# Kernel tuning notes

Hardware: AMD Instinct MI355X
Metric: run time of the kernel (lower is better)

The kernel has to match this reference:

```python
import jax, jax.numpy as jnp
import numpy as np

NHEAD = 8
TOPKS = [16, 8]  # coarse -> fine (indexed by loop i over reversed pyramids)


def _gather_kv(t, idx):
    # t: [b, M, nh, d], idx: [b, N, K, nh] -> gathered [b, N, K, nh, d]
    b, M, nh, d = t.shape
    bi = jnp.arange(b)[:, None, None, None]
    hi = jnp.arange(nh)[None, None, None, :]
    return t[bi, idx, hi]


def _process_level(query, key, value, topk_pos, topk_prev, topk):
    # query: [b, c, h0, w0]; key/value: [b, c, h1, w1] with h1=h0, w1=w0
    bs, c, h0, w0 = query.shape
    _, _, h1, w1 = key.shape
    nh = NHEAD
    d = c // nh
    N = (h0 // 2) * (w0 // 2)
    # b c h w -> b (h w) nh d
    k = key.reshape(bs, c, h1 * w1).transpose(0, 2, 1).reshape(bs, h1 * w1, nh, d)
    v = value.reshape(bs, c, h1 * w1).transpose(0, 2, 1).reshape(bs, h1 * w1, nh, d)
    # b c (h 2) (w 2) -> b (h w) 4 nh d  (2x2 query groups)
    q = query.reshape(bs, c, h0 // 2, 2, w0 // 2, 2)
    q = q.transpose(0, 2, 4, 3, 5, 1).reshape(bs, N, 4, nh, d)
    # expand each coarse candidate position into its 2x2 children in the key grid
    tp = topk_pos * 2  # [2, b, N, Kp, nh]
    idx = jnp.stack([(tp[0] + x) * w1 + (tp[1] + y)
                     for x in (0, 1) for y in (0, 1)], axis=3)  # [b,N,Kp,4,nh]
    K = topk_prev * 4
    idx = idx.reshape(bs, N, K, nh)
    # sparse scores: QK[b,n,t,k,h] = <q[b,n,t,h,:], key[b, idx[b,n,k,h], h, :]>
    kg = _gather_kv(k, idx)  # [b,N,K,nh,d]
    QK = jnp.einsum('bnthd,bnkhd->bntkh', q, kg) * (d ** -0.5)
    A = jax.nn.softmax(QK, axis=-2)  # softmax over the K candidates
    # top-k over candidates (dim=-2 of A); lax.top_k works on last axis
    A_t = jnp.swapaxes(A, -1, -2)  # [b,N,4,nh,K]
    ts_t, li = jax.lax.top_k(A_t, topk)
    idx_bc = jnp.broadcast_to(jnp.swapaxes(idx, -1, -2)[:, :, None], A_t.shape)
    ti_t = jnp.take_along_axis(idx_bc, li, axis=-1)
    topk_score = jnp.swapaxes(ts_t, -1, -2)  # [b,N,4,topk,nh]
    topk_idx = jnp.swapaxes(ti_t, -1, -2)
    # value aggregation (idx is repeated over the 4 group slots in the original,
    # so a single gather is the same math): message[b,n,t,h,d]=sum_k A*v[idx]
    vg = _gather_kv(v, idx)  # [b,N,K,nh,d]
    message = jnp.einsum('bntkh,bnkhd->bnthd', A, vg)  # [b,N,4,nh,d]

    def regroup(x):  # b (h w) (t1 t2) k nh -> b (h t1 w t2) k nh
        x = x.reshape(bs, h0 // 2, w0 // 2, 2, 2, topk, nh)
        return x.transpose(0, 1, 3, 2, 4, 5, 6).reshape(bs, h0 * w0, topk, nh)

    return message, regroup(topk_score), regroup(topk_idx)


def _forward(q_fine, q_coarse, k_fine, k_coarse, v_fine, v_coarse, weight, topk_pos):
    queries = [q_fine, q_coarse]  # original list order: fine -> coarse
    keys = [k_fine, k_coarse]
    values = [v_fine, v_coarse]
    messages = []
    topk = TOPKS[0]
    tp = topk_pos
    for i, (q, k, v) in enumerate(zip(queries[::-1], keys[::-1], values[::-1])):
        w1 = k.shape[3]
        topk_prev, topk = topk, TOPKS[i]
        msg, ts, ti = _process_level(q, k, v, tp, topk_prev, topk)
        messages.append(msg)
        tp = jnp.stack([ti // w1, ti % w1])  # (row, col) in current key grid
    wsm = jax.nn.softmax(weight)

    def comb(x, H):  # b (H W) (t1 t2) h d -> b (H t1 W t2) h d, t1=t2=2
        bs, N, _, nh, d = x.shape
        W = N // H
        x = x.reshape(bs, H, W, 2, 2, nh, d).transpose(0, 1, 3, 2, 4, 5, 6)
        return x.reshape(bs, H * 2 * W * 2, nh, d)

    fm = None
    for i, m in enumerate(messages):
        if i == 0:
            fm = m * wsm[i]
        else:
            fm = fm[:, :, None] + m * wsm[i]
        # faithful to original: queries[-i] (note queries[-0] == queries[0])
        H = queries[-i].shape[2]
        fm = comb(fm, H)
    return fm  # [b, Hf*Wf, nh, d]


def setup_inputs() -> dict:
    key = jax.random.key(0)
    ks = jax.random.split(key, 8)
    f = jnp.float32
    return {
        'q_fine': jax.random.normal(ks[0], (2, 128, 128, 128), f),
        'q_coarse': jax.random.normal(ks[1], (2, 128, 64, 64), f),
        'k_fine': jax.random.normal(ks[2], (2, 128, 128, 128), f),
        'k_coarse': jax.random.normal(ks[3], (2, 128, 64, 64), f),
        'v_fine': jax.random.normal(ks[4], (2, 128, 128, 128), f),
        'v_coarse': jax.random.normal(ks[5], (2, 128, 64, 64), f),
        'weight': jax.random.normal(ks[6], (2,), f),
        'topk_pos': jax.random.randint(ks[7], (2, 2, 1024, 16, 8), 0, 32, dtype=jnp.int32),
    }


def reference(q_fine, q_coarse, k_fine, k_coarse, v_fine, v_coarse, weight, topk_pos):
    return _forward(q_fine, q_coarse, k_fine, k_coarse, v_fine, v_coarse, weight, topk_pos)
```

## Files before the change

kernel.cpp:

```cpp
#include <hip/hip_runtime.h>

#define C 128

__device__ __forceinline__ void wave_sync() {
  __builtin_amdgcn_wave_barrier();
  asm volatile("s_waitcnt lgkmcnt(0)" ::: "memory");
  __builtin_amdgcn_wave_barrier();
}

__device__ __forceinline__ void transpose_tile(const float* __restrict__ in,
                                               float* __restrict__ out, int P,
                                               int tx, int chHalf, int b,
                                               float (*tile)[65]) {
  int posBase = tx * 64;
  int chBase  = chHalf * 64;
  int tid = threadIdx.x;
  int lp = tid & 63;
  int lr = tid >> 6;
  const float* ip = in + (size_t)b * C * P;
  float* op = out + (size_t)b * C * P;
#pragma unroll
  for (int it = 0; it < 16; ++it) {
    int ch = lr + it * 4;
    tile[ch][lp] = ip[(size_t)(chBase + ch) * P + posBase + lp];
  }
  __syncthreads();
  int ch2 = chBase + lp;
  int hh = ch2 >> 4, dd = ch2 & 15;
#pragma unroll
  for (int it = 0; it < 16; ++it) {
    int pl = lr + it * 4;
    op[((size_t)hh * P + posBase + pl) * 16 + dd] = tile[lp][pl];
  }
}

__global__ __launch_bounds__(256) void transpose_coarse(
    const float* __restrict__ q, const float* __restrict__ k,
    const float* __restrict__ v, float* __restrict__ qo,
    float* __restrict__ ko, float* __restrict__ vo) {
  __shared__ alignas(16) float tile[64][65];
  int idx = blockIdx.x;
  int tx = idx & 63;
  int ty = (idx >> 6) % 6;
  int tz = idx / 384;
  int sel = ty >> 1;
  const float* in = sel == 0 ? q : sel == 1 ? k : v;
  float* out      = sel == 0 ? qo : sel == 1 ? ko : vo;
  transpose_tile(in, out, 4096, tx, ty & 1, tz, tile);
}

__global__ __launch_bounds__(256) void fused_mid(
    const float* __restrict__ qf, const float* __restrict__ kf,
    const float* __restrict__ vf, float* __restrict__ qtf,
    float* __restrict__ ktf, float* __restrict__ vtf,
    const float* __restrict__ qt, const float* __restrict__ kt,
    const float* __restrict__ vt, const int* __restrict__ parents,
    float* __restrict__ mc, int* __restrict__ ti_out)
{
  __shared__ alignas(16) float lds[64 * 65];

  if (blockIdx.x < 3072) {
    int idx = blockIdx.x;
    int tx = idx & 255;
    int ty = (idx >> 8) % 6;
    int tz = idx / 1536;
    int sel = ty >> 1;
    const float* in = sel == 0 ? qf : sel == 1 ? kf : vf;
    float* out      = sel == 0 ? qtf : sel == 1 ? ktf : vtf;
    transpose_tile(in, out, 16384, tx, ty & 1, tz, (float (*)[65])lds);
    return;
  }

  float (*als_t)[4][64]    = (float (*)[4][64])   lds;
  float (*als_k)[4][17][4] = (float (*)[4][17][4])(lds + 1024);
  float (*qls)[4][16]      = (float (*)[4][16])  (lds + 2112);
  int   (*cofs)[64]        = (int (*)[64])       (lds + 2368);

  const int abid = blockIdx.x - 3072;
  const int lane = threadIdx.x & 63;
  const int wid  = threadIdx.x >> 6;
  const int wg = (abid & 7) * 512 + (abid >> 3);
  const int u  = wg * 4 + wid;
  const int h  = u & 7;
  const int bn = u >> 3;
  const int n  = bn & 1023;
  const int b  = bn >> 10;
  const int hb = n >> 5;
  const int wb = n & 31;
  const int hD = h * 16;
  const int bh = b * 8 + h;

  { int t = lane >> 4, dd = lane & 15;
    int pix = (hb * 2 + (t >> 1)) * 64 + (wb * 2 + (t & 1));
    qls[wid][t][dd] = qt[((size_t)bh * 4096 + pix) * 16 + dd]; }
  int cand, off0;
  { int kp = lane >> 2, c = lane & 3;
    int r  = parents[(size_t)b * 131072          + n * 128 + kp * 8 + h];
    int cc = parents[(size_t)b * 131072 + 262144 + n * 128 + kp * 8 + h];
    cand = (2 * r + (c >> 1)) * 64 + 2 * cc + (c & 1);
    off0 = (bh * 4096 + cand) * 16;
    cofs[wid][lane] = off0; }
  wave_sync();

  const float4* kv4 = (const float4*)(kt + off0);
  float4 k0 = kv4[0], k1 = kv4[1], k2 = kv4[2], k3 = kv4[3];
  float sc[4];
#pragma unroll
  for (int t = 0; t < 4; ++t) {
    const float4* qv = (const float4*)qls[wid][t];
    float4 q0 = qv[0], q1 = qv[1], q2 = qv[2], q3 = qv[3];
    float acc = k0.x*q0.x + k0.y*q0.y + k0.z*q0.z + k0.w*q0.w
              + k1.x*q1.x + k1.y*q1.y + k1.z*q1.z + k1.w*q1.w
              + k2.x*q2.x + k2.y*q2.y + k2.z*q2.z + k2.w*q2.w
              + k3.x*q3.x + k3.y*q3.y + k3.z*q3.z + k3.w*q3.w;
    sc[t] = acc * 0.25f;
  }

  float mx[4], ex[4], sm[4], a[4];
#pragma unroll
  for (int t = 0; t < 4; ++t) mx[t] = sc[t];
#pragma unroll
  for (int off = 32; off >= 1; off >>= 1)
#pragma unroll
    for (int t = 0; t < 4; ++t) mx[t] = fmaxf(mx[t], __shfl_xor(mx[t], off));
#pragma unroll
  for (int t = 0; t < 4; ++t) { ex[t] = __expf(sc[t] - mx[t]); sm[t] = ex[t]; }
#pragma unroll
  for (int off = 32; off >= 1; off >>= 1)
#pragma unroll
    for (int t = 0; t < 4; ++t) sm[t] += __shfl_xor(sm[t], off);
#pragma unroll
  for (int t = 0; t < 4; ++t) { a[t] = ex[t] / sm[t]; als_t[wid][t][lane] = a[t]; }
  *(float4*)&als_k[wid][lane >> 4][lane & 15][0] = make_float4(a[0], a[1], a[2], a[3]);
  wave_sync();

#pragma unroll
  for (int tt = 0; tt < 4; ++tt) {
    float myv = a[tt];
    int rank = 0;
    for (int j4 = 0; j4 < 64; j4 += 4) {
      float4 vj = *(const float4*)&als_t[wid][tt][j4];
      rank += (vj.x > myv) || (vj.x == myv && (j4 + 0) < lane);
      rank += (vj.y > myv) || (vj.y == myv && (j4 + 1) < lane);
      rank += (vj.z > myv) || (vj.z == myv && (j4 + 2) < lane);
      rank += (vj.w > myv) || (vj.w == myv && (j4 + 3) < lane);
    }
    if (rank < 16) {
      int n1 = (2 * hb + (tt >> 1)) * 64 + 2 * wb + (tt & 1);
      ti_out[((size_t)bh * 4096 + n1) * 16 + rank] = cand;
    }
  }

  {
    const int g = lane >> 4, dd = lane & 15;
    float acc0 = 0.f, acc1 = 0.f, acc2 = 0.f, acc3 = 0.f;
#pragma unroll
    for (int k4 = 0; k4 < 16; k4 += 4) {
      int4 cv = *(const int4*)&cofs[wid][g * 16 + k4];
      float4 a0 = *(const float4*)&als_k[wid][g][k4 + 0][0];
      float4 a1 = *(const float4*)&als_k[wid][g][k4 + 1][0];
      float4 a2 = *(const float4*)&als_k[wid][g][k4 + 2][0];
      float4 a3 = *(const float4*)&als_k[wid][g][k4 + 3][0];
      float v0 = vt[cv.x + dd];
      float v1 = vt[cv.y + dd];
      float v2 = vt[cv.z + dd];
      float v3 = vt[cv.w + dd];
      acc0 += a0.x * v0; acc1 += a0.y * v0; acc2 += a0.z * v0; acc3 += a0.w * v0;
      acc0 += a1.x * v1; acc1 += a1.y * v1; acc2 += a1.z * v1; acc3 += a1.w * v1;
      acc0 += a2.x * v2; acc1 += a2.y * v2; acc2 += a2.z * v2; acc3 += a2.w * v2;
      acc0 += a3.x * v3; acc1 += a3.y * v3; acc2 += a3.z * v3; acc3 += a3.w * v3;
    }
    acc0 += __shfl_xor(acc0, 16); acc0 += __shfl_xor(acc0, 32);
    acc1 += __shfl_xor(acc1, 16); acc1 += __shfl_xor(acc1, 32);
    acc2 += __shfl_xor(acc2, 16); acc2 += __shfl_xor(acc2, 32);
    acc3 += __shfl_xor(acc3, 16); acc3 += __shfl_xor(acc3, 32);
    float msg = (g & 2) ? ((g & 1) ? acc3 : acc2) : ((g & 1) ? acc1 : acc0);
    int m = hb * 128 + (wb >> 3) * 32 + (g >> 1) * 16 + (wb & 7) * 2 + (g & 1);
    mc[(b * 4096 + m) * C + hD + dd] = msg;
  }
}

__global__ __launch_bounds__(256) void attn_fine2(
    const float* __restrict__ qt, const float* __restrict__ kt,
    const float* __restrict__ vt, const int* __restrict__ tin,
    const float* __restrict__ mc, const float* __restrict__ weight,
    float* __restrict__ out)
{
  __shared__ alignas(16) float als_k[4][2][4][17][4];
  __shared__ alignas(16) float qls[4][2][4][16];
  __shared__ alignas(16) int   cofs[4][2][64];

  const int lane = threadIdx.x & 63;
  const int wid  = threadIdx.x >> 6;
  const int wg = (blockIdx.x & 7) * 1024 + (blockIdx.x >> 3);
  const int p  = wg * 4 + wid;
  const int wb2 = p & 31;
  const int hb  = (p >> 5) & 63;
  const int h   = (p >> 11) & 7;
  const int b   = p >> 14;
  const int bh  = b * 8 + h;
  const int nA  = hb * 64 + wb2 * 2;
  const int hD  = h * 16;

  { int t = lane >> 4, dd = lane & 15;
    int rowq = (hb * 2 + (t >> 1)) * 128;
    qls[wid][0][t][dd] = qt[((size_t)bh * 16384 + rowq + wb2 * 4     + (t & 1)) * 16 + dd];
    qls[wid][1][t][dd] = qt[((size_t)bh * 16384 + rowq + wb2 * 4 + 2 + (t & 1)) * 16 + dd];
  }
  int off0A, off0B;
  { int kp = lane >> 2, c = lane & 3;
    int tA = tin[((size_t)bh * 4096 + nA    ) * 16 + kp];
    int tB = tin[((size_t)bh * 4096 + nA + 1) * 16 + kp];
    int candA = (2 * (tA >> 6) + (c >> 1)) * 128 + 2 * (tA & 63) + (c & 1);
    int candB = (2 * (tB >> 6) + (c >> 1)) * 128 + 2 * (tB & 63) + (c & 1);
    off0A = (bh * 16384 + candA) * 16;
    off0B = (bh * 16384 + candB) * 16;
    cofs[wid][0][lane] = off0A;
    cofs[wid][1][lane] = off0B;
  }
  wave_sync();

  float4 kA0, kA1, kA2, kA3, kB0, kB1, kB2, kB3;
  { const float4* kv = (const float4*)(kt + off0A); kA0 = kv[0]; kA1 = kv[1]; kA2 = kv[2]; kA3 = kv[3]; }
  { const float4* kv = (const float4*)(kt + off0B); kB0 = kv[0]; kB1 = kv[1]; kB2 = kv[2]; kB3 = kv[3]; }

  float ex0[4], ex1[4];
#pragma unroll
  for (int t = 0; t < 4; ++t) {
    { const float4* qv = (const float4*)qls[wid][0][t];
      float4 q0 = qv[0], q1 = qv[1], q2 = qv[2], q3 = qv[3];
      float acc = kA0.x*q0.x + kA0.y*q0.y + kA0.z*q0.z + kA0.w*q0.w
                + kA1.x*q1.x + kA1.y*q1.y + kA1.z*q1.z + kA1.w*q1.w
                + kA2.x*q2.x + kA2.y*q2.y + kA2.z*q2.z + kA2.w*q2.w
                + kA3.x*q3.x + kA3.y*q3.y + kA3.z*q3.z + kA3.w*q3.w;
      ex0[t] = __expf(acc * 0.25f); }
    { const float4* qv = (const float4*)qls[wid][1][t];
      float4 q0 = qv[0], q1 = qv[1], q2 = qv[2], q3 = qv[3];
      float acc = kB0.x*q0.x + kB0.y*q0.y + kB0.z*q0.z + kB0.w*q0.w
                + kB1.x*q1.x + kB1.y*q1.y + kB1.z*q1.z + kB1.w*q1.w
                + kB2.x*q2.x + kB2.y*q2.y + kB2.z*q2.z + kB2.w*q2.w
                + kB3.x*q3.x + kB3.y*q3.y + kB3.z*q3.z + kB3.w*q3.w;
      ex1[t] = __expf(acc * 0.25f); }
  }
  *(float4*)&als_k[wid][0][lane >> 4][lane & 15][0] = make_float4(ex0[0], ex0[1], ex0[2], ex0[3]);
  *(float4*)&als_k[wid][1][lane >> 4][lane & 15][0] = make_float4(ex1[0], ex1[1], ex1[2], ex1[3]);
  wave_sync();

  const int g = lane >> 4, dd = lane & 15;
  float mcvA = mc[((size_t)b * 4096 + nA    ) * C + hD + dd];
  float mcvB = mc[((size_t)b * 4096 + nA + 1) * C + hD + dd];

  float smA[4], smB[4];
#pragma unroll
  for (int t = 0; t < 4; ++t) { smA[t] = ex0[t]; smB[t] = ex1[t]; }
#pragma unroll
  for (int off = 32; off >= 1; off >>= 1)
#pragma unroll
    for (int t = 0; t < 4; ++t) {
      smA[t] += __shfl_xor(smA[t], off);
      smB[t] += __shfl_xor(smB[t], off);
    }

  float aA0 = 0, aA1 = 0, aA2 = 0, aA3 = 0;
  float aB0 = 0, aB1 = 0, aB2 = 0, aB3 = 0;
#pragma unroll
  for (int k4 = 0; k4 < 16; k4 += 4) {
    int4 cvA = *(const int4*)&cofs[wid][0][g * 16 + k4];
    int4 cvB = *(const int4*)&cofs[wid][1][g * 16 + k4];
    float vA0 = vt[cvA.x + dd], vA1 = vt[cvA.y + dd];
    float vA2 = vt[cvA.z + dd], vA3 = vt[cvA.w + dd];
    float vB0 = vt[cvB.x + dd], vB1 = vt[cvB.y + dd];
    float vB2 = vt[cvB.z + dd], vB3 = vt[cvB.w + dd];
    float4 wA0 = *(const float4*)&als_k[wid][0][g][k4 + 0][0];
    float4 wA1 = *(const float4*)&als_k[wid][0][g][k4 + 1][0];
    float4 wA2 = *(const float4*)&als_k[wid][0][g][k4 + 2][0];
    float4 wA3 = *(const float4*)&als_k[wid][0][g][k4 + 3][0];
    float4 wB0 = *(const float4*)&als_k[wid][1][g][k4 + 0][0];
    float4 wB1 = *(const float4*)&als_k[wid][1][g][k4 + 1][0];
    float4 wB2 = *(const float4*)&als_k[wid][1][g][k4 + 2][0];
    float4 wB3 = *(const float4*)&als_k[wid][1][g][k4 + 3][0];
    aA0 += wA0.x * vA0; aA1 += wA0.y * vA0; aA2 += wA0.z * vA0; aA3 += wA0.w * vA0;
    aA0 += wA1.x * vA1; aA1 += wA1.y * vA1; aA2 += wA1.z * vA1; aA3 += wA1.w * vA1;
    aA0 += wA2.x * vA2; aA1 += wA2.y * vA2; aA2 += wA2.z * vA2; aA3 += wA2.w * vA2;
    aA0 += wA3.x * vA3; aA1 += wA3.y * vA3; aA2 += wA3.z * vA3; aA3 += wA3.w * vA3;
    aB0 += wB0.x * vB0; aB1 += wB0.y * vB0; aB2 += wB0.z * vB0; aB3 += wB0.w * vB0;
    aB0 += wB1.x * vB1; aB1 += wB1.y * vB1; aB2 += wB1.z * vB1; aB3 += wB1.w * vB1;
    aB0 += wB2.x * vB2; aB1 += wB2.y * vB2; aB2 += wB2.z * vB2; aB3 += wB2.w * vB2;
    aB0 += wB3.x * vB3; aB1 += wB3.y * vB3; aB2 += wB3.z * vB3; aB3 += wB3.w * vB3;
  }
  aA0 += __shfl_xor(aA0, 16); aA0 += __shfl_xor(aA0, 32);
  aA1 += __shfl_xor(aA1, 16); aA1 += __shfl_xor(aA1, 32);
  aA2 += __shfl_xor(aA2, 16); aA2 += __shfl_xor(aA2, 32);
  aA3 += __shfl_xor(aA3, 16); aA3 += __shfl_xor(aA3, 32);
  aB0 += __shfl_xor(aB0, 16); aB0 += __shfl_xor(aB0, 32);
  aB1 += __shfl_xor(aB1, 16); aB1 += __shfl_xor(aB1, 32);
  aB2 += __shfl_xor(aB2, 16); aB2 += __shfl_xor(aB2, 32);
  aB3 += __shfl_xor(aB3, 16); aB3 += __shfl_xor(aB3, 32);

  float msgA = (g & 2) ? ((g & 1) ? aA3 : aA2) : ((g & 1) ? aA1 : aA0);
  float msgB = (g & 2) ? ((g & 1) ? aB3 : aB2) : ((g & 1) ? aB1 : aB0);
  float smvA = (g & 2) ? ((g & 1) ? smA[3] : smA[2]) : ((g & 1) ? smA[1] : smA[0]);
  float smvB = (g & 2) ? ((g & 1) ? smB[3] : smB[2]) : ((g & 1) ? smB[1] : smB[0]);
  msgA /= smvA;
  msgB /= smvB;

  float w0 = weight[0], w1 = weight[1];
  float wm = fmaxf(w0, w1);
  float e0 = __expf(w0 - wm), e1 = __expf(w1 - wm);
  float inv = 1.0f / (e0 + e1);
  int rowq = (hb * 2 + (g >> 1)) * 128;
  out[((size_t)b * 16384 + rowq + wb2 * 4     + (g & 1)) * C + hD + dd] =
      (e0 * inv) * mcvA + (e1 * inv) * msgA;
  out[((size_t)b * 16384 + rowq + wb2 * 4 + 2 + (g & 1)) * C + hD + dd] =
      (e0 * inv) * mcvB + (e1 * inv) * msgB;
}

extern "C" void kernel_launch(void* const* d_in, const int* in_sizes, int n_in,
                              void* d_out, int out_size, void* d_ws, size_t ws_size,
                              hipStream_t stream) {
  const float* q_fine   = (const float*)d_in[0];
  const float* q_coarse = (const float*)d_in[1];
  const float* k_fine   = (const float*)d_in[2];
  const float* k_coarse = (const float*)d_in[3];
  const float* v_fine   = (const float*)d_in[4];
  const float* v_coarse = (const float*)d_in[5];
  const float* weight   = (const float*)d_in[6];
  const int*   topk_pos = (const int*)d_in[7];
  float* out = (float*)d_out;

  const int PF = 16384, PC = 4096;
  float* ws   = (float*)d_ws;
  float* qt_f = ws;
  float* kt_f = qt_f + 2 * PF * C;
  float* vt_f = kt_f + 2 * PF * C;
  float* qt_c = vt_f + 2 * PF * C;
  float* kt_c = qt_c + 2 * PC * C;
  float* vt_c = kt_c + 2 * PC * C;
  float* mc   = vt_c + 2 * PC * C;
  int*   ti   = (int*)(mc + 2 * 4096 * C);

  dim3 blk(256);
  transpose_coarse<<<768, blk, 0, stream>>>(q_coarse, k_coarse, v_coarse,
                                            qt_c, kt_c, vt_c);
  fused_mid<<<3072 + 4096, blk, 0, stream>>>(q_fine, k_fine, v_fine,
                                             qt_f, kt_f, vt_f,
                                             qt_c, kt_c, vt_c, topk_pos, mc, ti);
  attn_fine2<<<8192, blk, 0, stream>>>(qt_f, kt_f, vt_f, ti, mc, weight, out);
}
```

Measured before the change: 112.5 us.

## Split fused mid kernel and process two coarse queries per wave

```diff
diff --git a/kernel.cpp b/kernel.cpp
--- a/kernel.cpp
+++ b/kernel.cpp
@@ -49,134 +49,190 @@
   transpose_tile(in, out, 4096, tx, ty & 1, tz, tile);
 }
 
-__global__ __launch_bounds__(256) void fused_mid(
-    const float* __restrict__ qf, const float* __restrict__ kf,
-    const float* __restrict__ vf, float* __restrict__ qtf,
-    float* __restrict__ ktf, float* __restrict__ vtf,
+__global__ __launch_bounds__(256) void transpose_fine(
+    const float* __restrict__ q, const float* __restrict__ k,
+    const float* __restrict__ v, float* __restrict__ qo,
+    float* __restrict__ ko, float* __restrict__ vo) {
+  __shared__ alignas(16) float tile[64][65];
+  int idx = blockIdx.x;
+  int tx = idx & 255;
+  int ty = (idx >> 8) % 6;
+  int tz = idx / 1536;
+  int sel = ty >> 1;
+  const float* in = sel == 0 ? q : sel == 1 ? k : v;
+  float* out      = sel == 0 ? qo : sel == 1 ? ko : vo;
+  transpose_tile(in, out, 16384, tx, ty & 1, tz, tile);
+}
+
+__global__ __launch_bounds__(256) void attn_coarse2(
     const float* __restrict__ qt, const float* __restrict__ kt,
     const float* __restrict__ vt, const int* __restrict__ parents,
     float* __restrict__ mc, int* __restrict__ ti_out)
 {
-  __shared__ alignas(16) float lds[64 * 65];
-
-  if (blockIdx.x < 3072) {
-    int idx = blockIdx.x;
-    int tx = idx & 255;
-    int ty = (idx >> 8) % 6;
-    int tz = idx / 1536;
-    int sel = ty >> 1;
-    const float* in = sel == 0 ? qf : sel == 1 ? kf : vf;
-    float* out      = sel == 0 ? qtf : sel == 1 ? ktf : vtf;
-    transpose_tile(in, out, 16384, tx, ty & 1, tz, (float (*)[65])lds);
-    return;
-  }
-
-  float (*als_t)[4][64]    = (float (*)[4][64])   lds;
-  float (*als_k)[4][17][4] = (float (*)[4][17][4])(lds + 1024);
-  float (*qls)[4][16]      = (float (*)[4][16])  (lds + 2112);
-  int   (*cofs)[64]        = (int (*)[64])       (lds + 2368);
-
-  const int abid = blockIdx.x - 3072;
+  __shared__ alignas(16) float als_t[4][2][4][64];
+  __shared__ alignas(16) float als_k[4][2][4][17][4];
+  __shared__ alignas(16) float qls[4][2][4][16];
+  __shared__ alignas(16) int   cofs[4][2][64];
+
   const int lane = threadIdx.x & 63;
   const int wid  = threadIdx.x >> 6;
-  const int wg = (abid & 7) * 512 + (abid >> 3);
-  const int u  = wg * 4 + wid;
-  const int h  = u & 7;
-  const int bn = u >> 3;
-  const int n  = bn & 1023;
-  const int b  = bn >> 10;
-  const int hb = n >> 5;
-  const int wb = n & 31;
-  const int hD = h * 16;
-  const int bh = b * 8 + h;
+  const int wg = (blockIdx.x & 7) * 256 + (blockIdx.x >> 3);
+  const int p  = wg * 4 + wid;
+  const int wb2 = p & 15;
+  const int hb  = (p >> 4) & 31;
+  const int h   = (p >> 9) & 7;
+  const int b   = p >> 12;
+  const int bh  = b * 8 + h;
+  const int hD  = h * 16;
+  const int wbA = wb2 * 2, wbB = wbA + 1;
+  const int nA  = hb * 32 + wbA;
 
   { int t = lane >> 4, dd = lane & 15;
-    int pix = (hb * 2 + (t >> 1)) * 64 + (wb * 2 + (t & 1));
-    qls[wid][t][dd] = qt[((size_t)bh * 4096 + pix) * 16 + dd]; }
-  int cand, off0;
+    int row = (hb * 2 + (t >> 1)) * 64;
+    int colA = wbA * 2 + (t & 1);
+    qls[wid][0][t][dd] = qt[((size_t)bh * 4096 + row + colA    ) * 16 + dd];
+    qls[wid][1][t][dd] = qt[((size_t)bh * 4096 + row + colA + 2) * 16 + dd];
+  }
+  int candA, candB, offA, offB;
   { int kp = lane >> 2, c = lane & 3;
-    int r  = parents[(size_t)b * 131072          + n * 128 + kp * 8 + h];
-    int cc = parents[(size_t)b * 131072 + 262144 + n * 128 + kp * 8 + h];
-    cand = (2 * r + (c >> 1)) * 64 + 2 * cc + (c & 1);
-    off0 = (bh * 4096 + cand) * 16;
-    cofs[wid][lane] = off0; }
+    size_t baseR = (size_t)b * 131072 + kp * 8 + h;
+    int rA = parents[baseR           + (size_t)nA * 128];
+    int cA = parents[baseR + 262144  + (size_t)nA * 128];
+    int rB = parents[baseR           + (size_t)(nA + 1) * 128];
+    int cB = parents[baseR + 262144  + (size_t)(nA + 1) * 128];
+    candA = (2 * rA + (c >> 1)) * 64 + 2 * cA + (c & 1);
+    candB = (2 * rB + (c >> 1)) * 64 + 2 * cB + (c & 1);
+    offA = (bh * 4096 + candA) * 16;
+    offB = (bh * 4096 + candB) * 16;
+    cofs[wid][0][lane] = offA;
+    cofs[wid][1][lane] = offB;
+  }
   wave_sync();
 
-  const float4* kv4 = (const float4*)(kt + off0);
-  float4 k0 = kv4[0], k1 = kv4[1], k2 = kv4[2], k3 = kv4[3];
-  float sc[4];
+  float4 kA0, kA1, kA2, kA3, kB0, kB1, kB2, kB3;
+  { const float4* kv = (const float4*)(kt + offA); kA0 = kv[0]; kA1 = kv[1]; kA2 = kv[2]; kA3 = kv[3]; }
+  { const float4* kv = (const float4*)(kt + offB); kB0 = kv[0]; kB1 = kv[1]; kB2 = kv[2]; kB3 = kv[3]; }
+
+  float scA[4], scB[4];
 #pragma unroll
   for (int t = 0; t < 4; ++t) {
-    const float4* qv = (const float4*)qls[wid][t];
-    float4 q0 = qv[0], q1 = qv[1], q2 = qv[2], q3 = qv[3];
-    float acc = k0.x*q0.x + k0.y*q0.y + k0.z*q0.z + k0.w*q0.w
-              + k1.x*q1.x + k1.y*q1.y + k1.z*q1.z + k1.w*q1.w
-              + k2.x*q2.x + k2.y*q2.y + k2.z*q2.z + k2.w*q2.w
-              + k3.x*q3.x + k3.y*q3.y + k3.z*q3.z + k3.w*q3.w;
-    sc[t] = acc * 0.25f;
-  }
-
-  float mx[4], ex[4], sm[4], a[4];
-#pragma unroll
-  for (int t = 0; t < 4; ++t) mx[t] = sc[t];
+    { const float4* qv = (const float4*)qls[wid][0][t];
+      float4 q0 = qv[0], q1 = qv[1], q2 = qv[2], q3 = qv[3];
+      float acc = kA0.x*q0.x + kA0.y*q0.y + kA0.z*q0.z + kA0.w*q0.w
+                + kA1.x*q1.x + kA1.y*q1.y + kA1.z*q1.z + kA1.w*q1.w
+                + kA2.x*q2.x + kA2.y*q2.y + kA2.z*q2.z + kA2.w*q2.w
+                + kA3.x*q3.x + kA3.y*q3.y + kA3.z*q3.z + kA3.w*q3.w;
+      scA[t] = acc * 0.25f; }
+    { const float4* qv = (const float4*)qls[wid][1][t];
+      float4 q0 = qv[0], q1 = qv[1], q2 = qv[2], q3 = qv[3];
+      float acc = kB0.x*q0.x + kB0.y*q0.y + kB0.z*q0.z + kB0.w*q0.w
+                + kB1.x*q1.x + kB1.y*q1.y + kB1.z*q1.z + kB1.w*q1.w
+                + kB2.x*q2.x + kB2.y*q2.y + kB2.z*q2.z + kB2.w*q2.w
+                + kB3.x*q3.x + kB3.y*q3.y + kB3.z*q3.z + kB3.w*q3.w;
+      scB[t] = acc * 0.25f; }
+  }
+
+  float mxA[4], mxB[4], exA[4], exB[4], smA[4], smB[4], aA[4], aB[4];
+#pragma unroll
+  for (int t = 0; t < 4; ++t) { mxA[t] = scA[t]; mxB[t] = scB[t]; }
 #pragma unroll
   for (int off = 32; off >= 1; off >>= 1)
 #pragma unroll
-    for (int t = 0; t < 4; ++t) mx[t] = fmaxf(mx[t], __shfl_xor(mx[t], off));
-#pragma unroll
-  for (int t = 0; t < 4; ++t) { ex[t] = __expf(sc[t] - mx[t]); sm[t] = ex[t]; }
+    for (int t = 0; t < 4; ++t) {
+      mxA[t] = fmaxf(mxA[t], __shfl_xor(mxA[t], off));
+      mxB[t] = fmaxf(mxB[t], __shfl_xor(mxB[t], off));
+    }
+#pragma unroll
+  for (int t = 0; t < 4; ++t) {
+    exA[t] = __expf(scA[t] - mxA[t]); smA[t] = exA[t];
+    exB[t] = __expf(scB[t] - mxB[t]); smB[t] = exB[t];
+  }
 #pragma unroll
   for (int off = 32; off >= 1; off >>= 1)
 #pragma unroll
-    for (int t = 0; t < 4; ++t) sm[t] += __shfl_xor(sm[t], off);
-#pragma unroll
-  for (int t = 0; t < 4; ++t) { a[t] = ex[t] / sm[t]; als_t[wid][t][lane] = a[t]; }
-  *(float4*)&als_k[wid][lane >> 4][lane & 15][0] = make_float4(a[0], a[1], a[2], a[3]);
+    for (int t = 0; t < 4; ++t) {
+      smA[t] += __shfl_xor(smA[t], off);
+      smB[t] += __shfl_xor(smB[t], off);
+    }
+#pragma unroll
+  for (int t = 0; t < 4; ++t) {
+    aA[t] = exA[t] / smA[t]; als_t[wid][0][t][lane] = aA[t];
+    aB[t] = exB[t] / smB[t]; als_t[wid][1][t][lane] = aB[t];
+  }
+  *(float4*)&als_k[wid][0][lane >> 4][lane & 15][0] = make_float4(aA[0], aA[1], aA[2], aA[3]);
+  *(float4*)&als_k[wid][1][lane >> 4][lane & 15][0] = make_float4(aB[0], aB[1], aB[2], aB[3]);
   wave_sync();
 
 #pragma unroll
   for (int tt = 0; tt < 4; ++tt) {
-    float myv = a[tt];
-    int rank = 0;
+    float mvA = aA[tt], mvB = aB[tt];
+    int rkA = 0, rkB = 0;
     for (int j4 = 0; j4 < 64; j4 += 4) {
-      float4 vj = *(const float4*)&als_t[wid][tt][j4];
-      rank += (vj.x > myv) || (vj.x == myv && (j4 + 0) < lane);
-      rank += (vj.y > myv) || (vj.y == myv && (j4 + 1) < lane);
-      rank += (vj.z > myv) || (vj.z == myv && (j4 + 2) < lane);
-      rank += (vj.w > myv) || (vj.w == myv && (j4 + 3) < lane);
-    }
-    if (rank < 16) {
-      int n1 = (2 * hb + (tt >> 1)) * 64 + 2 * wb + (tt & 1);
-      ti_out[((size_t)bh * 4096 + n1) * 16 + rank] = cand;
+      float4 vA = *(const float4*)&als_t[wid][0][tt][j4];
+      float4 vB = *(const float4*)&als_t[wid][1][tt][j4];
+      rkA += (vA.x > mvA) || (vA.x == mvA && (j4 + 0) < lane);
+      rkB += (vB.x > mvB) || (vB.x == mvB && (j4 + 0) < lane);
+      rkA += (vA.y > mvA) || (vA.y == mvA && (j4 + 1) < lane);
+      rkB += (vB.y > mvB) || (vB.y == mvB && (j4 + 1) < lane);
+      rkA += (vA.z > mvA) || (vA.z == mvA && (j4 + 2) < lane);
+      rkB += (vB.z > mvB) || (vB.z == mvB && (j4 + 2) < lane);
+      rkA += (vA.w > mvA) || (vA.w == mvA && (j4 + 3) < lane);
+      rkB += (vB.w > mvB) || (vB.w == mvB && (j4 + 3) < lane);
+    }
+    int rowT = 2 * hb + (tt >> 1);
+    if (rkA < 16) {
+      int n1 = rowT * 64 + 2 * wbA + (tt & 1);
+      ti_out[((size_t)bh * 4096 + n1) * 16 + rkA] = candA;
+    }
+    if (rkB < 16) {
+      int n1 = rowT * 64 + 2 * wbB + (tt & 1);
+      ti_out[((size_t)bh * 4096 + n1) * 16 + rkB] = candB;
     }
   }
 
   {
     const int g = lane >> 4, dd = lane & 15;
-    float acc0 = 0.f, acc1 = 0.f, acc2 = 0.f, acc3 = 0.f;
+    float aA0 = 0, aA1 = 0, aA2 = 0, aA3 = 0;
+    float aB0 = 0, aB1 = 0, aB2 = 0, aB3 = 0;
 #pragma unroll
     for (int k4 = 0; k4 < 16; k4 += 4) {
-      int4 cv = *(const int4*)&cofs[wid][g * 16 + k4];
-      float4 a0 = *(const float4*)&als_k[wid][g][k4 + 0][0];
-      float4 a1 = *(const float4*)&als_k[wid][g][k4 + 1][0];
-      float4 a2 = *(const float4*)&als_k[wid][g][k4 + 2][0];
-      float4 a3 = *(const float4*)&als_k[wid][g][k4 + 3][0];
-      float v0 = vt[cv.x + dd];
-      float v1 = vt[cv.y + dd];
-      float v2 = vt[cv.z + dd];
-      float v3 = vt[cv.w + dd];
-      acc0 += a0.x * v0; acc1 += a0.y * v0; acc2 += a0.z * v0; acc3 += a0.w * v0;
-      acc0 += a1.x * v1; acc1 += a1.y * v1; acc2 += a1.z * v1; acc3 += a1.w * v1;
-      acc0 += a2.x * v2; acc1 += a2.y * v2; acc2 += a2.z * v2; acc3 += a2.w * v2;
-      acc0 += a3.x * v3; acc1 += a3.y * v3; acc2 += a3.z * v3; acc3 += a3.w * v3;
-    }
-    acc0 += __shfl_xor(acc0, 16); acc0 += __shfl_xor(acc0, 32);
-    acc1 += __shfl_xor(acc1, 16); acc1 += __shfl_xor(acc1, 32);
-    acc2 += __shfl_xor(acc2, 16); acc2 += __shfl_xor(acc2, 32);
-    acc3 += __shfl_xor(acc3, 16); acc3 += __shfl_xor(acc3, 32);
-    float msg = (g & 2) ? ((g & 1) ? acc3 : acc2) : ((g & 1) ? acc1 : acc0);
-    int m = hb * 128 + (wb >> 3) * 32 + (g >> 1) * 16 + (wb & 7) * 2 + (g & 1);
-    mc[(b * 4096 + m) * C + hD + dd] = msg;
+      int4 cvA = *(const int4*)&cofs[wid][0][g * 16 + k4];
+      int4 cvB = *(const int4*)&cofs[wid][1][g * 16 + k4];
+      float vA0 = vt[cvA.x + dd], vA1 = vt[cvA.y + dd];
+      float vA2 = vt[cvA.z + dd], vA3 = vt[cvA.w + dd];
+      float vB0 = vt[cvB.x + dd], vB1 = vt[cvB.y + dd];
+      float vB2 = vt[cvB.z + dd], vB3 = vt[cvB.w + dd];
+      float4 wA0 = *(const float4*)&als_k[wid][0][g][k4 + 0][0];
+      float4 wA1 = *(const float4*)&als_k[wid][0][g][k4 + 1][0];
+      float4 wA2 = *(const float4*)&als_k[wid][0][g][k4 + 2][0];
+      float4 wA3 = *(const float4*)&als_k[wid][0][g][k4 + 3][0];
+      float4 wB0 = *(const float4*)&als_k[wid][1][g][k4 + 0][0];
+      float4 wB1 = *(const float4*)&als_k[wid][1][g][k4 + 1][0];
+      float4 wB2 = *(const float4*)&als_k[wid][1][g][k4 + 2][0];
+      float4 wB3 = *(const float4*)&als_k[wid][1][g][k4 + 3][0];
+      aA0 += wA0.x * vA0; aA1 += wA0.y * vA0; aA2 += wA0.z * vA0; aA3 += wA0.w * vA0;
+      aA0 += wA1.x * vA1; aA1 += wA1.y * vA1; aA2 += wA1.z * vA1; aA3 += wA1.w * vA1;
+      aA0 += wA2.x * vA2; aA1 += wA2.y * vA2; aA2 += wA2.z * vA2; aA3 += wA2.w * vA2;
+      aA0 += wA3.x * vA3; aA1 += wA3.y * vA3; aA2 += wA3.z * vA3; aA3 += wA3.w * vA3;
+      aB0 += wB0.x * vB0; aB1 += wB0.y * vB0; aB2 += wB0.z * vB0; aB3 += wB0.w * vB0;
+      aB0 += wB1.x * vB1; aB1 += wB1.y * vB1; aB2 += wB1.z * vB1; aB3 += wB1.w * vB1;
+      aB0 += wB2.x * vB2; aB1 += wB2.y * vB2; aB2 += wB2.z * vB2; aB3 += wB2.w * vB2;
+      aB0 += wB3.x * vB3; aB1 += wB3.y * vB3; aB2 += wB3.z * vB3; aB3 += wB3.w * vB3;
+    }
+    aA0 += __shfl_xor(aA0, 16); aA0 += __shfl_xor(aA0, 32);
+    aA1 += __shfl_xor(aA1, 16); aA1 += __shfl_xor(aA1, 32);
+    aA2 += __shfl_xor(aA2, 16); aA2 += __shfl_xor(aA2, 32);
+    aA3 += __shfl_xor(aA3, 16); aA3 += __shfl_xor(aA3, 32);
+    aB0 += __shfl_xor(aB0, 16); aB0 += __shfl_xor(aB0, 32);
+    aB1 += __shfl_xor(aB1, 16); aB1 += __shfl_xor(aB1, 32);
+    aB2 += __shfl_xor(aB2, 16); aB2 += __shfl_xor(aB2, 32);
+    aB3 += __shfl_xor(aB3, 16); aB3 += __shfl_xor(aB3, 32);
+    float msgA = (g & 2) ? ((g & 1) ? aA3 : aA2) : ((g & 1) ? aA1 : aA0);
+    float msgB = (g & 2) ? ((g & 1) ? aB3 : aB2) : ((g & 1) ? aB1 : aB0);
+    int mA = hb * 128 + (wbA >> 3) * 32 + (g >> 1) * 16 + (wbA & 7) * 2 + (g & 1);
+    int mB = hb * 128 + (wbB >> 3) * 32 + (g >> 1) * 16 + (wbB & 7) * 2 + (g & 1);
+    mc[(b * 4096 + mA) * C + hD + dd] = msgA;
+    mc[(b * 4096 + mB) * C + hD + dd] = msgB;
   }
 }
 
@@ -342,8 +398,8 @@
   dim3 blk(256);
   transpose_coarse<<<768, blk, 0, stream>>>(q_coarse, k_coarse, v_coarse,
                                             qt_c, kt_c, vt_c);
-  fused_mid<<<3072 + 4096, blk, 0, stream>>>(q_fine, k_fine, v_fine,
-                                             qt_f, kt_f, vt_f,
-                                             qt_c, kt_c, vt_c, topk_pos, mc, ti);
+  attn_coarse2<<<2048, blk, 0, stream>>>(qt_c, kt_c, vt_c, topk_pos, mc, ti);
+  transpose_fine<<<3072, blk, 0, stream>>>(q_fine, k_fine, v_fine,
+                                           qt_f, kt_f, vt_f);
   attn_fine2<<<8192, blk, 0, stream>>>(qt_f, kt_f, vt_f, ti, mc, weight, out);
 }
```

New measurement: 130.4 us. +15.9%, slower.
